# Kernel optimization log

Hardware: AMD Instinct MI355X
Metric: run time of the kernel (lower is better)

## Reference

```python
import jax, jax.numpy as jnp
import numpy as np

V, E, H = 50257, 256, 256   # vocab/output_size, embed_size, hidden_size
T, B = 4096, 64             # encoder time steps, batch


def setup_inputs() -> dict:
    key = jax.random.key(0)
    ks = jax.random.split(key, 12)
    s = 0.05
    return {
        "input_ids": jax.random.randint(ks[0], (B,), 0, V),
        "hidden": jax.random.normal(ks[1], (1, B, H), dtype=jnp.float32) * s,
        "encoder_outputs": jax.random.normal(ks[2], (T, B, 2 * H), dtype=jnp.float32) * s,
        # learned parameters (PyTorch Linear convention: W @ x.T, W shape (out, in))
        "emb": jax.random.normal(ks[3], (V, E), dtype=jnp.float32) * s,
        "W_attn": jax.random.normal(ks[4], (H, 3 * H), dtype=jnp.float32) * s,
        "b_attn": jnp.zeros((H,), jnp.float32),
        "v": jax.random.normal(ks[5], (H,), dtype=jnp.float32) * s,
        "W_comb": jax.random.normal(ks[6], (H, 2 * H + E), dtype=jnp.float32) * s,
        "b_comb": jnp.zeros((H,), jnp.float32),
        "W_ih": jax.random.normal(ks[7], (3 * H, H), dtype=jnp.float32) * s,
        "W_hh": jax.random.normal(ks[8], (3 * H, H), dtype=jnp.float32) * s,
        "b_ih": jnp.zeros((3 * H,), jnp.float32),
        "b_hh": jnp.zeros((3 * H,), jnp.float32),
        "W_out": jax.random.normal(ks[9], (V, 3 * H), dtype=jnp.float32) * s,
        "b_out": jnp.zeros((V,), jnp.float32),
    }


def reference(input_ids, hidden, encoder_outputs, emb, W_attn, b_attn, v,
              W_comb, b_comb, W_ih, W_hh, b_ih, b_hh, W_out, b_out):
    Tn, Bn, _ = encoder_outputs.shape
    Hn = hidden.shape[-1]
    embedded = emb[input_ids]                 # (B, E)
    h0 = hidden[0]                            # (B, H)

    # additive (Bahdanau) attention: energies over time axis
    h_rep = jnp.broadcast_to(h0[None], (Tn, Bn, Hn))            # (T, B, H)
    cat = jnp.concatenate([h_rep, encoder_outputs], axis=2)     # (T, B, 3H)
    energies = jnp.tanh(cat @ W_attn.T + b_attn)                # (T, B, H)
    scores = jnp.einsum('tbh,h->tb', energies, v)               # (T, B)
    attn = jax.nn.softmax(scores, axis=0)                       # softmax over time
    context = jnp.einsum('tb,tbd->bd', attn, encoder_outputs)   # (B, 2H)

    # combine context with embedded input
    comb = jnp.concatenate([context, embedded], axis=1) @ W_comb.T + b_comb  # (B, H)

    # single GRU step (PyTorch gate order: r, z, n)
    gx = comb @ W_ih.T + b_ih                 # (B, 3H)
    gh = h0 @ W_hh.T + b_hh                   # (B, 3H)
    xr, xz, xn = jnp.split(gx, 3, axis=1)
    hr, hz, hn = jnp.split(gh, 3, axis=1)
    r = jax.nn.sigmoid(xr + hr)
    z = jax.nn.sigmoid(xz + hz)
    n = jnp.tanh(xn + r * hn)
    h_new = (1.0 - z) * n + z * h0            # (B, H)

    logits = jnp.concatenate([h_new, context], axis=1) @ W_out.T + b_out  # (B, V)
    logp = jax.nn.log_softmax(logits, axis=1)
    return logp, h_new[None]                  # hidden_i shape (1, B, H)
```

## Files before the change

kernel.cpp:

```cpp
#include <hip/hip_runtime.h>
#include <hip/hip_bf16.h>
#include <cstdint>
#include <cstddef>

#define Tn 4096
#define Bn 64
#define Hn 256
#define En 256
#define Vn 50257
#define D2H 512
#define K3H 768

typedef __attribute__((ext_vector_type(8))) short short8;
typedef __attribute__((ext_vector_type(4))) float f32x4;

__device__ __forceinline__ short bfs(float f)
{
    __hip_bfloat16 h = __float2bfloat16(f);
    return *reinterpret_cast<short*>(&h);
}

__device__ __forceinline__ short8 pack8(const float4 x0, const float4 x1)
{
    short8 r;
    r[0] = bfs(x0.x); r[1] = bfs(x0.y); r[2] = bfs(x0.z); r[3] = bfs(x0.w);
    r[4] = bfs(x1.x); r[5] = bfs(x1.y); r[6] = bfs(x1.z); r[7] = bfs(x1.w);
    return r;
}

__device__ __forceinline__ uint2 pack4(const float4 v)
{
    uint2 r;
    r.x = (unsigned)(unsigned short)bfs(v.x) | ((unsigned)(unsigned short)bfs(v.y) << 16);
    r.y = (unsigned)(unsigned short)bfs(v.z) | ((unsigned)(unsigned short)bfs(v.w) << 16);
    return r;
}

__device__ __forceinline__ float bf2f(unsigned short u)
{
    return __uint_as_float(((unsigned)u) << 16);
}


__global__ __launch_bounds__(256) void k1_embed_base(
    const int* __restrict__ ids, const float* __restrict__ hidden,
    const float* __restrict__ emb, const float* __restrict__ W_attn,
    const float* __restrict__ b_attn,
    float* __restrict__ baseB, float* __restrict__ emb_g)
{
    const int b = blockIdx.x, h = threadIdx.x;
    __shared__ float h0[Hn];
    h0[h] = hidden[b * Hn + h];
    __syncthreads();
    float acc = b_attn[h];
    const float* wrow = W_attn + (size_t)h * K3H;
#pragma unroll 8
    for (int k = 0; k < Hn; ++k) acc += wrow[k] * h0[k];
    baseB[b * Hn + h] = acc;
    const int id = ids[b];
    emb_g[b * En + h] = emb[(size_t)id * En + h];
}

__global__ __launch_bounds__(64) void k1b_w2frag(
    const float* __restrict__ W_attn, unsigned short* __restrict__ w2frag)
{
    const int blk = blockIdx.x;
    const int nt = blk >> 4, kb = blk & 15;
    const int l = threadIdx.x, lr = l & 15, lg = l >> 4;
    const int h = nt * 16 + lr;
    const float* src = W_attn + (size_t)h * K3H + Hn + kb * 32 + lg * 8;
    float4 x0 = *reinterpret_cast<const float4*>(src);
    float4 x1 = *reinterpret_cast<const float4*>(src + 4);
    reinterpret_cast<short8*>(w2frag)[(size_t)blk * 64 + l] = pack8(x0, x1);
}

__global__ __launch_bounds__(512, 2) void k2f_attn(
    const float* __restrict__ enc, const unsigned short* __restrict__ w2frag,
    const float* __restrict__ vvec, const float* __restrict__ baseB,
    float* __restrict__ part, float2* __restrict__ meta)
{
    const int tid = threadIdx.x;
    const int bx  = blockIdx.x;
    const int b   = bx & 63;
    const int cid = bx >> 6;
    const int l = tid & 63;
    const int w = tid >> 6;
    const int mh = w >> 2;
    const int ns = w & 3;
    const int lr = l & 15, lg = l >> 4;

    __shared__ unsigned short abf[64][520];
    __shared__ float red[64][5];
    __shared__ float wts[64];

    const float* gbase = enc + ((size_t)(cid * 64 + w * 8 + lg) * Bn + b) * D2H
                       + lr * 4;

#define LOADREG(dst, c) do {                                                  \
    _Pragma("unroll")                                                         \
    for (int u = 0; u < 2; ++u)                                               \
        dst[u] = *reinterpret_cast<const float4*>(                            \
            gbase + (size_t)u * 131072 + (c) * 64);                           \
    } while (0)

#define WRITEC(src, c) do {                                                   \
    _Pragma("unroll")                                                         \
    for (int u = 0; u < 2; ++u)                                               \
        *reinterpret_cast<uint2*>(&abf[w * 8 + u * 4 + lg][(c) * 64 + lr * 4])\
            = pack4(src[u]);                                                  \
    } while (0)

    {
        float4 st0[2], st1[2];
#pragma unroll 1
        for (int kc = 0; kc < 8; kc += 2) {
            LOADREG(st0, kc);
            LOADREG(st1, kc + 1);
            WRITEC(st0, kc);
            WRITEC(st1, kc + 1);
        }
    }
    __syncthreads();

    f32x4 acc[2][4];
    const f32x4 zero = {0.f, 0.f, 0.f, 0.f};
#pragma unroll
    for (int mi = 0; mi < 2; ++mi)
#pragma unroll
        for (int ni = 0; ni < 4; ++ni) acc[mi][ni] = zero;

    const short8* wf = reinterpret_cast<const short8*>(w2frag);

#pragma unroll
    for (int kb = 0; kb < 16; ++kb) {
        short8 bfr[4];
#pragma unroll
        for (int ni = 0; ni < 4; ++ni)
            bfr[ni] = wf[(size_t)(((ns * 4 + ni) * 16) + kb) * 64 + l];
#pragma unroll
        for (int mi = 0; mi < 2; ++mi) {
            short8 a = *reinterpret_cast<const short8*>(
                &abf[mh * 32 + mi * 16 + lr][kb * 32 + lg * 8]);
#pragma unroll
            for (int ni = 0; ni < 4; ++ni)
                acc[mi][ni] = __builtin_amdgcn_mfma_f32_16x16x32_bf16(
                    a, bfr[ni], acc[mi][ni], 0, 0, 0);
        }
    }
#undef LOADREG
#undef WRITEC

    float psum[2][4];
#pragma unroll
    for (int mi = 0; mi < 2; ++mi)
#pragma unroll
        for (int r = 0; r < 4; ++r) psum[mi][r] = 0.f;
#pragma unroll
    for (int ni = 0; ni < 4; ++ni) {
        const int h = ns * 64 + ni * 16 + lr;
        const float vh = vvec[h];
        const float bt = baseB[b * Hn + h];
#pragma unroll
        for (int mi = 0; mi < 2; ++mi)
#pragma unroll
            for (int r = 0; r < 4; ++r)
                psum[mi][r] += vh * tanhf(acc[mi][ni][r] + bt);
    }
#pragma unroll
    for (int d = 1; d < 16; d <<= 1)
#pragma unroll
        for (int mi = 0; mi < 2; ++mi)
#pragma unroll
            for (int r = 0; r < 4; ++r)
                psum[mi][r] += __shfl_xor(psum[mi][r], d, 64);
    if (lr == 0) {
#pragma unroll
        for (int mi = 0; mi < 2; ++mi)
#pragma unroll
            for (int r = 0; r < 4; ++r)
                red[mh * 32 + mi * 16 + lg * 4 + r][ns] = psum[mi][r];
    }
    __syncthreads();

    if (tid < 64) {
        float s = red[tid][0] + red[tid][1] + red[tid][2] + red[tid][3];
        float m = s;
#pragma unroll
        for (int d = 1; d < 64; d <<= 1) m = fmaxf(m, __shfl_xor(m, d, 64));
        const float e = expf(s - m);
        float lsum = e;
#pragma unroll
        for (int d = 1; d < 64; d <<= 1) lsum += __shfl_xor(lsum, d, 64);
        wts[tid] = e;
        if (tid == 0) meta[bx] = make_float2(m, lsum);
    }
    __syncthreads();

    float c0 = 0.f;
#pragma unroll 4
    for (int t = 0; t < 64; ++t)
        c0 += wts[t] * bf2f(abf[t][tid]);
    part[(size_t)bx * 512 + tid] = c0;
}

__global__ __launch_bounds__(256) void k56_ctx_gru(
    const float* __restrict__ part, const float2* __restrict__ meta,
    const float* __restrict__ hidden, const float* __restrict__ emb_g,
    const float* __restrict__ W_comb, const float* __restrict__ b_comb,
    const float* __restrict__ W_ih, const float* __restrict__ W_hh,
    const float* __restrict__ b_ih, const float* __restrict__ b_hh,
    float* __restrict__ y, float* __restrict__ out_hidden)
{
    const int b = blockIdx.x, tid = threadIdx.x;
    __shared__ float sc[64];
    __shared__ float in_[K3H];
    __shared__ float h0[Hn];
    __shared__ float comb[Hn];
    __shared__ float gx[K3H], gh[K3H];
    if (tid < 64) {
        const float2 ml = meta[(size_t)tid * 64 + b];
        float M = ml.x;
#pragma unroll
        for (int d = 1; d < 64; d <<= 1) M = fmaxf(M, __shfl_xor(M, d, 64));
        const float e = expf(ml.x - M);
        float L = e * ml.y;
#pragma unroll
        for (int d = 1; d < 64; d <<= 1) L += __shfl_xor(L, d, 64);
        sc[tid] = e / L;
    }
    in_[512 + tid] = emb_g[b * En + tid];
    h0[tid] = hidden[b * Hn + tid];
    __syncthreads();
    {
        const int d0 = tid * 2;
        float c0 = 0.f, c1 = 0.f;
#pragma unroll 4
        for (int c = 0; c < 64; ++c) {
            const float s = sc[c];
            const float2 p = *reinterpret_cast<const float2*>(
                part + ((size_t)c * 64 + b) * 512 + d0);
            c0 += s * p.x; c1 += s * p.y;
        }
        in_[d0] = c0; in_[d0 + 1] = c1;
        y[(size_t)b * K3H + Hn + d0]     = c0;
        y[(size_t)b * K3H + Hn + d0 + 1] = c1;
    }
    __syncthreads();
    {
        float c = b_comb[tid];
        const float* wr = W_comb + (size_t)tid * K3H;
#pragma unroll 8
        for (int k = 0; k < K3H; ++k) c += wr[k] * in_[k];
        comb[tid] = c;
    }
    __syncthreads();
#pragma unroll
    for (int p = 0; p < 3; ++p) {
        const int g = p * 256 + tid;
        float a = b_ih[g], bh = b_hh[g];
        const float* wi = W_ih + (size_t)g * Hn;
        const float* wh = W_hh + (size_t)g * Hn;
#pragma unroll 8
        for (int k = 0; k < Hn; ++k) { a += wi[k] * comb[k]; bh += wh[k] * h0[k]; }
        gx[g] = a; gh[g] = bh;
    }
    __syncthreads();
    const float r = 1.f / (1.f + expf(-(gx[tid] + gh[tid])));
    const float z = 1.f / (1.f + expf(-(gx[256 + tid] + gh[256 + tid])));
    const float n = tanhf(gx[512 + tid] + r * gh[512 + tid]);
    const float hn = (1.f - z) * n + z * h0[tid];
    y[(size_t)b * K3H + tid] = hn;
    out_hidden[b * Hn + tid] = hn;
}

__global__ __launch_bounds__(64) void k7y_pack(
    const float* __restrict__ y, unsigned short* __restrict__ yfrag)
{
    const int blk = blockIdx.x;
    const int ni = blk / 24, kb = blk % 24;
    const int l = threadIdx.x, lr = l & 15, lg = l >> 4;
    const int b = ni * 16 + lr;
    const float* src = y + (size_t)b * K3H + kb * 32 + lg * 8;
    float4 x0 = *reinterpret_cast<const float4*>(src);
    float4 x1 = *reinterpret_cast<const float4*>(src + 4);
    reinterpret_cast<short8*>(yfrag)[(size_t)blk * 64 + l] = pack8(x0, x1);
}

__global__ __launch_bounds__(256) void k7_logits(
    const float* __restrict__ W_out, const float* __restrict__ b_out,
    const unsigned short* __restrict__ yfrag, float* __restrict__ out)
{
    const int tid = threadIdx.x;
    const int vbase = blockIdx.x * 64;
    const int l = tid & 63, w = tid >> 6;
    const int lr = l & 15, lg = l >> 4;

    const short8* yf = reinterpret_cast<const short8*>(yfrag);

    f32x4 acc[4];
    const f32x4 zero = {0.f, 0.f, 0.f, 0.f};
#pragma unroll
    for (int ni = 0; ni < 4; ++ni) acc[ni] = zero;

    int v = vbase + w * 16 + lr;
    if (v >= Vn) v = Vn - 1;
    const float* wrow = W_out + (size_t)v * K3H + lg * 8;

#pragma unroll 4
    for (int kb = 0; kb < 24; ++kb) {
        float4 x0 = *reinterpret_cast<const float4*>(wrow + kb * 32);
        float4 x1 = *reinterpret_cast<const float4*>(wrow + kb * 32 + 4);
        short8 a = pack8(x0, x1);
#pragma unroll
        for (int ni = 0; ni < 4; ++ni) {
            short8 bf = yf[(size_t)(ni * 24 + kb) * 64 + l];
            acc[ni] = __builtin_amdgcn_mfma_f32_16x16x32_bf16(
                a, bf, acc[ni], 0, 0, 0);
        }
    }

    __shared__ float lt[64][65];
#pragma unroll
    for (int ni = 0; ni < 4; ++ni)
#pragma unroll
        for (int r = 0; r < 4; ++r)
            lt[w * 16 + lg * 4 + r][ni * 16 + lr] = acc[ni][r];
    __syncthreads();

#pragma unroll
    for (int u = 0; u < 16; ++u) {
        const int idx = tid + u * 256;
        const int bb = idx >> 6, vv = idx & 63;
        const int vo = vbase + vv;
        if (vo < Vn)
            out[(size_t)bb * Vn + vo] = lt[vv][bb] + b_out[vo];
    }
}

#define VQ 12565

__global__ __launch_bounds__(1024) void k8a_partial(
    const float* __restrict__ out, float2* __restrict__ qmeta)
{
    const int b = blockIdx.x, q = blockIdx.y;
    const int lo = q * VQ, hi = (lo + VQ < Vn) ? lo + VQ : Vn;
    const float* row = out + (size_t)b * Vn;
    __shared__ float red[1024];
    float m = -1e30f;
    for (int i = lo + threadIdx.x; i < hi; i += 1024) m = fmaxf(m, row[i]);
    red[threadIdx.x] = m; __syncthreads();
    for (int s = 512; s > 0; s >>= 1) {
        if (threadIdx.x < s) red[threadIdx.x] = fmaxf(red[threadIdx.x], red[threadIdx.x + s]);
        __syncthreads();
    }
    m = red[0]; __syncthreads();
    float l = 0.f;
    for (int i = lo + threadIdx.x; i < hi; i += 1024) l += expf(row[i] - m);
    red[threadIdx.x] = l; __syncthreads();
    for (int s = 512; s > 0; s >>= 1) {
        if (threadIdx.x < s) red[threadIdx.x] += red[threadIdx.x + s];
        __syncthreads();
    }
    if (threadIdx.x == 0) qmeta[b * 4 + q] = make_float2(m, red[0]);
}

__global__ __launch_bounds__(1024) void k8b_apply(
    float* __restrict__ out, const float2* __restrict__ qmeta)
{
    const int b = blockIdx.x, q = blockIdx.y;
    const int lo = q * VQ, hi = (lo + VQ < Vn) ? lo + VQ : Vn;
    float2 q0 = qmeta[b * 4 + 0], q1 = qmeta[b * 4 + 1];
    float2 q2 = qmeta[b * 4 + 2], q3 = qmeta[b * 4 + 3];
    const float M = fmaxf(fmaxf(q0.x, q1.x), fmaxf(q2.x, q3.x));
    const float L = q0.y * expf(q0.x - M) + q1.y * expf(q1.x - M)
                  + q2.y * expf(q2.x - M) + q3.y * expf(q3.x - M);
    const float off = M + logf(L);
    float* row = out + (size_t)b * Vn;
    for (int i = lo + threadIdx.x; i < hi; i += 1024) row[i] -= off;
}

extern "C" void kernel_launch(void* const* d_in, const int* in_sizes, int n_in,
                              void* d_out, int out_size, void* d_ws, size_t ws_size,
                              hipStream_t stream)
{
    const int*   ids    = (const int*)d_in[0];
    const float* hidden = (const float*)d_in[1];
    const float* enc    = (const float*)d_in[2];
    const float* emb    = (const float*)d_in[3];
    const float* W_attn = (const float*)d_in[4];
    const float* b_attn = (const float*)d_in[5];
    const float* vvec   = (const float*)d_in[6];
    const float* W_comb = (const float*)d_in[7];
    const float* b_comb = (const float*)d_in[8];
    const float* W_ih   = (const float*)d_in[9];
    const float* W_hh   = (const float*)d_in[10];
    const float* b_ih   = (const float*)d_in[11];
    const float* b_hh   = (const float*)d_in[12];
    const float* W_out  = (const float*)d_in[13];
    const float* b_out  = (const float*)d_in[14];

    float* out = (float*)d_out;
    float* ws = (float*)d_ws;
    float*  baseB = ws;
    float*  emb_g = ws + 16384;
    float2* meta  = (float2*)(ws + 32768);
    float*  part  = ws + 40960;
    float*  y     = ws + 2138112;
    unsigned short* w2frag = (unsigned short*)(ws + 2187264);
    unsigned short* yfrag  = (unsigned short*)(ws + 2252800);
    float2* qmeta = (float2*)(ws + 2277376);

    hipLaunchKernelGGL(k1_embed_base, dim3(Bn), dim3(256), 0, stream,
                       ids, hidden, emb, W_attn, b_attn, baseB, emb_g);
    hipLaunchKernelGGL(k1b_w2frag, dim3(256), dim3(64), 0, stream,
                       W_attn, w2frag);
    hipLaunchKernelGGL(k2f_attn, dim3(4096), dim3(512), 0, stream,
                       enc, w2frag, vvec, baseB, part, meta);
    hipLaunchKernelGGL(k56_ctx_gru, dim3(Bn), dim3(256), 0, stream,
                       part, meta, hidden, emb_g, W_comb, b_comb,
                       W_ih, W_hh, b_ih, b_hh, y, out + (size_t)Bn * Vn);
    hipLaunchKernelGGL(k7y_pack, dim3(96), dim3(64), 0, stream, y, yfrag);
    hipLaunchKernelGGL(k7_logits, dim3((Vn + 63) / 64), dim3(256), 0, stream,
                       W_out, b_out, yfrag, out);
    hipLaunchKernelGGL(k8a_partial, dim3(Bn, 4), dim3(1024), 0, stream,
                       out, qmeta);
    hipLaunchKernelGGL(k8b_apply, dim3(Bn, 4), dim3(1024), 0, stream,
                       out, qmeta);
}
```

Baseline: 347.6 us.

## Load encoder fragments directly into MFMA registers, skipping LDS staging

The encoder tile is no longer staged through shared memory with a block-wide barrier before the MFMA loop. Each wave now reads its own A fragments from global memory, converts them to bf16 in registers and feeds the MFMAs directly. One wave per column group still writes the tile to LDS for later use. Because four waves (one per ns value) cover the same rows, each encoder element is now read from global or cache several times instead of once, and each lane's reads are strided rather than coalesced.

```diff
diff --git a/kernel.cpp b/kernel.cpp
--- a/kernel.cpp
+++ b/kernel.cpp
@@ -25,14 +25,6 @@
     short8 r;
     r[0] = bfs(x0.x); r[1] = bfs(x0.y); r[2] = bfs(x0.z); r[3] = bfs(x0.w);
     r[4] = bfs(x1.x); r[5] = bfs(x1.y); r[6] = bfs(x1.z); r[7] = bfs(x1.w);
-    return r;
-}
-
-__device__ __forceinline__ uint2 pack4(const float4 v)
-{
-    uint2 r;
-    r.x = (unsigned)(unsigned short)bfs(v.x) | ((unsigned)(unsigned short)bfs(v.y) << 16);
-    r.y = (unsigned)(unsigned short)bfs(v.z) | ((unsigned)(unsigned short)bfs(v.w) << 16);
     return r;
 }
 
@@ -89,39 +81,10 @@
     const int ns = w & 3;
     const int lr = l & 15, lg = l >> 4;
 
-    __shared__ unsigned short abf[64][520];
+    __shared__ unsigned short abf[64][528];
     __shared__ float red[64][5];
     __shared__ float wts[64];
 
-    const float* gbase = enc + ((size_t)(cid * 64 + w * 8 + lg) * Bn + b) * D2H
-                       + lr * 4;
-
-#define LOADREG(dst, c) do {                                                  \
-    _Pragma("unroll")                                                         \
-    for (int u = 0; u < 2; ++u)                                               \
-        dst[u] = *reinterpret_cast<const float4*>(                            \
-            gbase + (size_t)u * 131072 + (c) * 64);                           \
-    } while (0)
-
-#define WRITEC(src, c) do {                                                   \
-    _Pragma("unroll")                                                         \
-    for (int u = 0; u < 2; ++u)                                               \
-        *reinterpret_cast<uint2*>(&abf[w * 8 + u * 4 + lg][(c) * 64 + lr * 4])\
-            = pack4(src[u]);                                                  \
-    } while (0)
-
-    {
-        float4 st0[2], st1[2];
-#pragma unroll 1
-        for (int kc = 0; kc < 8; kc += 2) {
-            LOADREG(st0, kc);
-            LOADREG(st1, kc + 1);
-            WRITEC(st0, kc);
-            WRITEC(st1, kc + 1);
-        }
-    }
-    __syncthreads();
-
     f32x4 acc[2][4];
     const f32x4 zero = {0.f, 0.f, 0.f, 0.f};
 #pragma unroll
@@ -131,24 +94,41 @@
 
     const short8* wf = reinterpret_cast<const short8*>(w2frag);
 
+    const float* a0p = enc + ((size_t)(cid * 64 + mh * 32 + lr) * Bn + b) * D2H
+                     + lg * 8;
+    const float* a1p = a0p + (size_t)16 * Bn * D2H;
+    const bool wr_gate_base = true;
+
 #pragma unroll
     for (int kb = 0; kb < 16; ++kb) {
         short8 bfr[4];
 #pragma unroll
         for (int ni = 0; ni < 4; ++ni)
             bfr[ni] = wf[(size_t)(((ns * 4 + ni) * 16) + kb) * 64 + l];
-#pragma unroll
-        for (int mi = 0; mi < 2; ++mi) {
-            short8 a = *reinterpret_cast<const short8*>(
-                &abf[mh * 32 + mi * 16 + lr][kb * 32 + lg * 8]);
-#pragma unroll
-            for (int ni = 0; ni < 4; ++ni)
-                acc[mi][ni] = __builtin_amdgcn_mfma_f32_16x16x32_bf16(
-                    a, bfr[ni], acc[mi][ni], 0, 0, 0);
+
+        float4 x00 = *reinterpret_cast<const float4*>(a0p + kb * 32);
+        float4 x01 = *reinterpret_cast<const float4*>(a0p + kb * 32 + 4);
+        float4 x10 = *reinterpret_cast<const float4*>(a1p + kb * 32);
+        float4 x11 = *reinterpret_cast<const float4*>(a1p + kb * 32 + 4);
+        short8 A0 = pack8(x00, x01);
+        short8 A1 = pack8(x10, x11);
+
+        if (((kb ^ ns) & 3) == 0) {
+            *reinterpret_cast<short8*>(
+                &abf[mh * 32 + lr][kb * 32 + lg * 8]) = A0;
+            *reinterpret_cast<short8*>(
+                &abf[mh * 32 + 16 + lr][kb * 32 + lg * 8]) = A1;
         }
-    }
-#undef LOADREG
-#undef WRITEC
+
+#pragma unroll
+        for (int ni = 0; ni < 4; ++ni) {
+            acc[0][ni] = __builtin_amdgcn_mfma_f32_16x16x32_bf16(
+                A0, bfr[ni], acc[0][ni], 0, 0, 0);
+            acc[1][ni] = __builtin_amdgcn_mfma_f32_16x16x32_bf16(
+                A1, bfr[ni], acc[1][ni], 0, 0, 0);
+        }
+    }
+    (void)wr_gate_base;
 
     float psum[2][4];
 #pragma unroll
```

After: 478.2 us. +37.6%, slower.
